# Kernel optimization log

Hardware: AMD Instinct MI355X
Metric: run time of the kernel (lower is better)

## Reference

```python
import jax, jax.numpy as jnp
import numpy as np

B, S, D, H = 2, 2048, 1024, 16
HD = D // H  # head depth


def setup_inputs() -> dict:
    key = jax.random.key(0)
    ks = jax.random.split(key, 8)
    scale = 0.02
    K = jax.random.normal(ks[0], (B, S, D), jnp.float32)
    V = jax.random.normal(ks[1], (B, S, D), jnp.float32)
    Q = jax.random.normal(ks[2], (B, S, D), jnp.float32)
    # causal additive mask: 1.0 where attention is disallowed (strict upper triangle)
    mask = jnp.broadcast_to(
        jnp.triu(jnp.ones((S, S), jnp.float32), k=1)[None, None, :, :], (B, 1, S, S)
    )
    Wk = jax.random.normal(ks[3], (D, D), jnp.float32) * scale
    Wv = jax.random.normal(ks[4], (D, D), jnp.float32) * scale
    Wq = jax.random.normal(ks[5], (D, D), jnp.float32) * scale
    Wo = jax.random.normal(ks[6], (D, D), jnp.float32) * scale
    z = jnp.zeros((D,), jnp.float32)
    return {"K": K, "V": V, "Q": Q, "mask": mask,
            "Wk": Wk, "bk": z, "Wv": Wv, "bv": z,
            "Wq": Wq, "bq": z, "Wo": Wo, "bo": z}


def _split_heads(x):  # [B,S,D] -> [B,H,S,HD]
    return x.reshape(B, S, H, HD).transpose(0, 2, 1, 3)


def reference(K, V, Q, mask, Wk, bk, Wv, bv, Wq, bq, Wo, bo):
    k = _split_heads(K @ Wk + bk)
    v = _split_heads(V @ Wv + bv)
    q = _split_heads(Q @ Wq + bq)
    # NOTE: source scales by sqrt(d_model), not sqrt(head_depth)
    logits = jnp.einsum("bhqd,bhkd->bhqk", q, k) / jnp.sqrt(jnp.float32(D))
    logits = logits + mask * (-1e9)
    attn = jax.nn.softmax(logits, axis=-1)
    out = jnp.einsum("bhqk,bhkd->bhqd", attn, v)  # [B,H,S,HD]
    out = out.transpose(0, 2, 1, 3).reshape(B, S, D)
    return out @ Wo + bo
```

## Files before the change

### kernel.cpp

```cpp
#include <hip/hip_runtime.h>
#include <hip/hip_bf16.h>

typedef unsigned short u16;
typedef unsigned int u32;
typedef unsigned long long u64;
typedef __attribute__((ext_vector_type(8))) __bf16 bf16x8;
typedef __attribute__((ext_vector_type(4))) float f32x4;

#define SEQ 2048
#define DM 1024
#define NH 16
#define HDim 64

__device__ __forceinline__ float bf_lo(u32 u) { return __uint_as_float(u << 16); }
__device__ __forceinline__ float bf_hi(u32 u) { return __uint_as_float(u & 0xffff0000u); }
__device__ __forceinline__ u16 f2bf(float f) {
    u32 u = __float_as_uint(f);
    u32 r = (u + 0x7fffu + ((u >> 16) & 1u)) >> 16;
    return (u16)r;
}
__device__ __forceinline__ float bf2f(u16 h) { return __uint_as_float(((u32)h) << 16); }

__device__ __forceinline__ float fexp2(float x) {
#if __has_builtin(__builtin_amdgcn_exp2f)
    return __builtin_amdgcn_exp2f(x);
#else
    return __expf(x * 0.69314718056f);
#endif
}

__device__ __forceinline__ float frcp(float x) {
#if __has_builtin(__builtin_amdgcn_rcpf)
    return __builtin_amdgcn_rcpf(x);
#else
    return 1.0f / x;
#endif
}

__device__ __forceinline__ u32 merge2(u32 a, u32 b, float inv) {
    const float lo = (bf_lo(a) + bf_lo(b)) * inv;
    const float hi = (bf_hi(a) + bf_hi(b)) * inv;
    u32 r;
    asm("v_cvt_pk_bf16_f32 %0, %1, %2" : "=v"(r) : "v"(lo), "v"(hi));
    return r;
}

#define GLD16(g, l)                                                         \
    __builtin_amdgcn_global_load_lds(                                       \
        (const __attribute__((address_space(1))) void*)(g),                 \
        (__attribute__((address_space(3))) void*)(l), 16, 0, 0)

__device__ __forceinline__ bool detect_f32(const u32* q)
{
    const u32 w = q[threadIdx.x & 63];
    const int e0 = ((w & 0xffffu) >> 7) & 0xff;
    const int e1 = (w >> 23) & 0xff;
    const unsigned long long b = __ballot(e0 >= 0x90 || e1 >= 0x90);
    return b != 0ull;
}

__global__ __launch_bounds__(256)
void prep_all(const void* __restrict__ Qin, const void* __restrict__ Kin,
              const void* __restrict__ Vin,
              const void* __restrict__ w0, const void* __restrict__ w1,
              const void* __restrict__ w2, const void* __restrict__ w3,
              const void* __restrict__ b0, const void* __restrict__ b1,
              const void* __restrict__ b2, const void* __restrict__ b3,
              u16* __restrict__ Xall, u16* __restrict__ Wtall,
              u16* __restrict__ ball)
{
    __shared__ u16 T[64 * 66];
    const bool f = detect_f32((const u32*)Qin);
    const int t = threadIdx.x;
    const int bid = blockIdx.x;

    if (bid < 6144) {
        const int z = bid >> 11;
        const int bx = bid & 2047;
        const void* src = (z == 0) ? Qin : (z == 1) ? Kin : Vin;
        const size_t i0 = ((size_t)bx * 256 + t) * 8;
        u16* d = Xall + (size_t)z * 4194304 + i0;
        if (f) {
            const uint4* s = reinterpret_cast<const uint4*>((const float*)src + i0);
            uint4 a = s[0], b = s[1];
            u16 o[8];
            o[0] = f2bf(__uint_as_float(a.x)); o[1] = f2bf(__uint_as_float(a.y));
            o[2] = f2bf(__uint_as_float(a.z)); o[3] = f2bf(__uint_as_float(a.w));
            o[4] = f2bf(__uint_as_float(b.x)); o[5] = f2bf(__uint_as_float(b.y));
            o[6] = f2bf(__uint_as_float(b.z)); o[7] = f2bf(__uint_as_float(b.w));
            *reinterpret_cast<uint4*>(d) = *reinterpret_cast<const uint4*>(o);
        } else {
            *reinterpret_cast<uint4*>(d) =
                *reinterpret_cast<const uint4*>((const u16*)src + i0);
        }
    } else if (bid < 7168) {
        const int r = bid - 6144;
        const int z = r >> 8;
        const void* src = (z == 0) ? w0 : (z == 1) ? w1 : (z == 2) ? w2 : w3;
        const int n0 = ((r >> 4) & 15) * 64;
        const int k0 = (r & 15) * 64;
        const int c = t & 63, g = t >> 6;
        if (f) {
            const float* W = (const float*)src;
#pragma unroll
            for (int i = 0; i < 16; i++) {
                const int kl = g * 16 + i;
                T[kl * 66 + c] = f2bf(W[(size_t)(k0 + kl) * DM + n0 + c]);
            }
        } else {
            const u16* W = (const u16*)src;
#pragma unroll
            for (int i = 0; i < 16; i++) {
                const int kl = g * 16 + i;
                T[kl * 66 + c] = W[(size_t)(k0 + kl) * DM + n0 + c];
            }
        }
        __syncthreads();
        u16* dst = Wtall + (size_t)z * 1048576;
#pragma unroll
        for (int i = 0; i < 16; i++) {
            const int nl = g * 16 + i;
            dst[(size_t)(n0 + nl) * DM + k0 + c] = T[c * 66 + nl];
        }
    } else {
#pragma unroll
        for (int j = 0; j < 16; j++) {
            const int idx = t * 16 + j;
            const int z = idx >> 10, e = idx & 1023;
            const void* src = (z == 0) ? b0 : (z == 1) ? b1 : (z == 2) ? b2 : b3;
            ball[idx] = f ? f2bf(((const float*)src)[e]) : ((const u16*)src)[e];
        }
    }
}

__global__ __launch_bounds__(256)
void gemm128(const u16* __restrict__ Xall, const u16* __restrict__ Wtall,
             const u16* __restrict__ ball, u16* __restrict__ Yall)
{
    __shared__ __align__(16) u16 As[2][128 * 32];
    __shared__ __align__(16) u16 Bs[2][64 * 32];

    const int zz = blockIdx.z;
    const bool swp = (zz != 2);
    const u16* X  = Xall + (size_t)zz * 4194304;
    const u16* Wt = Wtall + (size_t)zz * 1048576;

    const int t    = threadIdx.x;
    const int w    = t >> 6;
    const int lane = t & 63;
    const int quad = lane >> 4;
    const int ln   = lane & 15;
    const int m0   = blockIdx.x * 128;
    const int n0   = blockIdx.y * 64;

    f32x4 acc[4][2];
#pragma unroll
    for (int i = 0; i < 4; i++)
#pragma unroll
        for (int j = 0; j < 2; j++) acc[i][j] = (f32x4){0.f, 0.f, 0.f, 0.f};

    const int swz = (lane >> 3) & 3;
    const u16* ag = X  + (size_t)(m0 + w * 32 + (lane >> 2)) * DM + ((lane & 3) ^ swz) * 8;
    const u16* bg = Wt + (size_t)(n0 + w * 16 + (lane >> 2)) * DM + ((lane & 3) ^ swz) * 8;

    const int wr = (w >> 1) * 64;
    const int wc = (w & 1) * 32;
    const int rs = (quad ^ ((ln >> 1) & 3)) * 8;

#define GSTAGE(B)                                        \
    {                                                    \
        GLD16(ag,           &As[B][w * 1024]);           \
        GLD16(ag + 16 * DM, &As[B][w * 1024 + 512]);     \
        GLD16(bg,           &Bs[B][w * 512]);            \
        ag += 32; bg += 32;                              \
    }

#define GCOMP(B)                                                              \
    {                                                                         \
        bf16x8 af[4], bfr[2];                                                 \
        _Pragma("unroll") for (int rt = 0; rt < 4; rt++)                      \
            af[rt] = *reinterpret_cast<const bf16x8*>(                        \
                &As[B][(wr + rt * 16 + ln) * 32 + rs]);                       \
        _Pragma("unroll") for (int ct = 0; ct < 2; ct++)                      \
            bfr[ct] = *reinterpret_cast<const bf16x8*>(                       \
                &Bs[B][(wc + ct * 16 + ln) * 32 + rs]);                       \
        if (swp) {                                                            \
            _Pragma("unroll") for (int rt = 0; rt < 4; rt++)                  \
                _Pragma("unroll") for (int ct = 0; ct < 2; ct++)              \
                    acc[rt][ct] = __builtin_amdgcn_mfma_f32_16x16x32_bf16(    \
                        bfr[ct], af[rt], acc[rt][ct], 0, 0, 0);               \
        } else {                                                              \
            _Pragma("unroll") for (int rt = 0; rt < 4; rt++)                  \
                _Pragma("unroll") for (int ct = 0; ct < 2; ct++)              \
                    acc[rt][ct] = __builtin_amdgcn_mfma_f32_16x16x32_bf16(    \
                        af[rt], bfr[ct], acc[rt][ct], 0, 0, 0);               \
        }                                                                     \
    }

    GSTAGE(0);
    __syncthreads();
#pragma unroll 1
    for (int it = 0; it < 15; ++it) {
        GSTAGE(1); GCOMP(0); __syncthreads();
        GSTAGE(0); GCOMP(1); __syncthreads();
    }
    GSTAGE(1); GCOMP(0); __syncthreads();
    GCOMP(1);
#undef GSTAGE
#undef GCOMP

    u16* Y = Yall + (size_t)zz * 4194304;

    if (swp) {
        const float scale = (zz == 0) ? 0.04508422f : 1.0f;
#pragma unroll
        for (int ct = 0; ct < 2; ct++) {
            const int nb = n0 + wc + ct * 16 + quad * 4;
            const int h = nb >> 6, hd = nb & (HDim - 1);
            float bv[4];
#pragma unroll
            for (int r = 0; r < 4; r++) bv[r] = bf2f(ball[zz * 1024 + nb + r]);
#pragma unroll
            for (int rt = 0; rt < 4; rt++) {
                const int m = m0 + wr + rt * 16 + ln;
                const int b = m >> 11, s = m & (SEQ - 1);
                u16 o4[4];
#pragma unroll
                for (int r = 0; r < 4; r++)
                    o4[r] = f2bf((acc[rt][ct][r] + bv[r]) * scale);
                *reinterpret_cast<u64*>(
                    Y + (((size_t)(b * NH + h)) * SEQ + s) * HDim + hd) =
                    *reinterpret_cast<const u64*>(o4);
            }
        }
    } else {
#pragma unroll
        for (int ct = 0; ct < 2; ct++) {
            const int n = n0 + wc + ct * 16 + ln;
            const float bv = bf2f(ball[zz * 1024 + n]);
            const int h = n >> 6, hd = n & (HDim - 1);
#pragma unroll
            for (int rt = 0; rt < 4; rt++) {
                const int m = m0 + wr + rt * 16 + quad * 4;
                const int b = m >> 11, s = m & (SEQ - 1);
                u16 o4[4];
#pragma unroll
                for (int r = 0; r < 4; r++) o4[r] = f2bf(acc[rt][ct][r] + bv);
                *reinterpret_cast<u64*>(
                    Y + (((size_t)(b * NH + h) * HDim + hd) * SEQ + s)) =
                    *reinterpret_cast<const u64*>(o4);
            }
        }
    }
}

__device__ __forceinline__ void attn_tile2(
    const u16* __restrict__ Ks, const u16* __restrict__ Vs,
    u16* __restrict__ Ps, const bf16x8& qf0, const bf16x8& qf1,
    int kt, int qrow, int w, int quad, int ln, f32x4* o, float& l,
    bool diag)
{
    f32x4 s[4];
    __builtin_amdgcn_s_setprio(1);
#pragma unroll
    for (int ct = 0; ct < 4; ct++) {
        const u16* kr = &Ks[(ct * 16 + ln) * 72 + quad * 8];
        bf16x8 kf0 = *reinterpret_cast<const bf16x8*>(kr);
        bf16x8 kf1 = *reinterpret_cast<const bf16x8*>(kr + 32);
        f32x4 z = (f32x4){0.f, 0.f, 0.f, 0.f};
        z = __builtin_amdgcn_mfma_f32_16x16x32_bf16(kf0, qf0, z, 0, 0, 0);
        s[ct] = __builtin_amdgcn_mfma_f32_16x16x32_bf16(kf1, qf1, z, 0, 0, 0);
    }
    __builtin_amdgcn_s_setprio(0);
    const int kb = kt * 64 + quad * 4;
    float lacc = 0.f;
#pragma unroll
    for (int ct = 0; ct < 4; ct++) {
        float e0 = fexp2(s[ct][0]);
        float e1 = fexp2(s[ct][1]);
        float e2 = fexp2(s[ct][2]);
        float e3 = fexp2(s[ct][3]);
        if (diag) {
            const int kc = kb + ct * 16;
            e0 = (kc + 0 <= qrow) ? e0 : 0.f;
            e1 = (kc + 1 <= qrow) ? e1 : 0.f;
            e2 = (kc + 2 <= qrow) ? e2 : 0.f;
            e3 = (kc + 3 <= qrow) ? e3 : 0.f;
        }
        lacc += (e0 + e1) + (e2 + e3);
        u32 pk[2];
        asm("v_cvt_pk_bf16_f32 %0, %1, %2" : "=v"(pk[0]) : "v"(e0), "v"(e1));
        asm("v_cvt_pk_bf16_f32 %0, %1, %2" : "=v"(pk[1]) : "v"(e2), "v"(e3));
        *reinterpret_cast<u64*>(&Ps[(w * 16 + ln) * 72 + ct * 16 + quad * 4]) =
            *reinterpret_cast<const u64*>(pk);
    }
    l += lacc;
    __builtin_amdgcn_s_setprio(1);
#pragma unroll
    for (int ks = 0; ks < 2; ks++) {
        bf16x8 pf = *reinterpret_cast<const bf16x8*>(
            &Ps[(w * 16 + ln) * 72 + ks * 32 + quad * 8]);
#pragma unroll
        for (int nt = 0; nt < 4; nt++) {
            bf16x8 vf = *reinterpret_cast<const bf16x8*>(
                &Vs[(nt * 16 + ln) * 72 + ks * 32 + quad * 8]);
            o[nt] = __builtin_amdgcn_mfma_f32_16x16x32_bf16(pf, vf, o[nt], 0, 0, 0);
        }
    }
    __builtin_amdgcn_s_setprio(0);
}

__global__ __launch_bounds__(256)
void attn_split(const u16* __restrict__ qh, const u16* __restrict__ kh,
                const u16* __restrict__ vt, u16* __restrict__ Opart,
                float* __restrict__ Lpart)
{
    __shared__ __align__(16) u16 Ks[64 * 72];
    __shared__ __align__(16) u16 Vs[64 * 72];
    __shared__ __align__(16) u16 Ps[64 * 72];

    const int t    = threadIdx.x;
    const int L    = blockIdx.x + 16 * (blockIdx.y + 32 * blockIdx.z);
    const int xcd  = L & 7;
    const int slot = L >> 3;
    const int bh   = xcd + 8 * (slot >> 5);
    const int rr   = slot & 31;
    const int i    = rr & 15;
    const int c    = rr >> 4;

    const int w    = t >> 6;
    const int lane = t & 63;
    const int quad = lane >> 4;
    const int ln   = lane & 15;
    const int qtH  = 31 - i;
    const int qtL  = i;
    const int m    = (i >= 8) ? 8 : 16 - i;
    const int kt0  = c ? m : 0;
    const int kt1  = c ? (qtH + 1) : m;

    const size_t kbase = (size_t)bh * SEQ * HDim;
    const size_t vbase = (size_t)bh * HDim * SEQ;

    const u16* qrH = qh + kbase + (size_t)(qtH * 64 + w * 16 + ln) * HDim;
    const bf16x8 qfH0 = *reinterpret_cast<const bf16x8*>(qrH + quad * 8);
    const bf16x8 qfH1 = *reinterpret_cast<const bf16x8*>(qrH + 32 + quad * 8);
    const u16* qrL = qh + kbase + (size_t)(qtL * 64 + w * 16 + ln) * HDim;
    const bf16x8 qfL0 = *reinterpret_cast<const bf16x8*>(qrL + quad * 8);
    const bf16x8 qfL1 = *reinterpret_cast<const bf16x8*>(qrL + 32 + quad * 8);

    f32x4 oH[4], oL[4];
    float lH = 0.f, lL = 0.f;
#pragma unroll
    for (int k = 0; k < 4; k++) {
        oH[k] = (f32x4){0.f, 0.f, 0.f, 0.f};
        oL[k] = (f32x4){0.f, 0.f, 0.f, 0.f};
    }

    const int srow = t >> 2;
    const int sc   = (t & 3) * 16;
    const int rowH = qtH * 64 + w * 16 + ln;
    const int rowL = qtL * 64 + w * 16 + ln;

    uint4 kr0, kr1, vr0, vr1;
    {
        const uint4* ksp = reinterpret_cast<const uint4*>(
            kh + kbase + (size_t)(kt0 * 64 + srow) * HDim + sc);
        kr0 = ksp[0]; kr1 = ksp[1];
        const uint4* vsp = reinterpret_cast<const uint4*>(
            vt + vbase + (size_t)srow * SEQ + kt0 * 64 + sc);
        vr0 = vsp[0]; vr1 = vsp[1];
    }

    for (int kt = kt0; kt < kt1; kt++) {
        {
            uint4* kd = reinterpret_cast<uint4*>(&Ks[srow * 72 + sc]);
            kd[0] = kr0; kd[1] = kr1;
            uint4* vd = reinterpret_cast<uint4*>(&Vs[srow * 72 + sc]);
            vd[0] = vr0; vd[1] = vr1;
        }
        __syncthreads();

        if (kt + 1 < kt1) {
            const uint4* ksp = reinterpret_cast<const uint4*>(
                kh + kbase + (size_t)((kt + 1) * 64 + srow) * HDim + sc);
            kr0 = ksp[0]; kr1 = ksp[1];
            const uint4* vsp = reinterpret_cast<const uint4*>(
                vt + vbase + (size_t)srow * SEQ + (kt + 1) * 64 + sc);
            vr0 = vsp[0]; vr1 = vsp[1];
            __builtin_amdgcn_sched_barrier(0);
        }

        attn_tile2(Ks, Vs, Ps, qfH0, qfH1, kt, rowH, w, quad, ln, oH, lH,
                   kt == qtH);
        if (kt <= qtL)
            attn_tile2(Ks, Vs, Ps, qfL0, qfL1, kt, rowL, w, quad, ln, oL, lL,
                       kt == qtL);

        __syncthreads();
    }

    lH += __shfl_xor(lH, 16); lH += __shfl_xor(lH, 32);
    lL += __shfl_xor(lL, 16); lL += __shfl_xor(lL, 32);

    const size_t cb = ((size_t)c * 32 + bh) * SEQ;
    if (lane < 16) {
        Lpart[cb + qtH * 64 + w * 16 + lane] = lH;
        Lpart[cb + qtL * 64 + w * 16 + lane] = lL;
    }
#pragma unroll
    for (int r = 0; r < 4; r++) {
        const int rH = qtH * 64 + w * 16 + quad * 4 + r;
        const int rL = qtL * 64 + w * 16 + quad * 4 + r;
        u16* dH = Opart + (cb + rH) * HDim + ln;
        u16* dL = Opart + (cb + rL) * HDim + ln;
#pragma unroll
        for (int nt = 0; nt < 4; nt++) {
            dH[nt * 16] = f2bf(oH[nt][r]);
            dL[nt * 16] = f2bf(oL[nt][r]);
        }
    }
}

__global__ __launch_bounds__(256)
void gemm_out(const u16* __restrict__ Opart, const float* __restrict__ Lpart,
              const u16* __restrict__ Wt, const u16* __restrict__ bias,
              void* __restrict__ dout, const u32* __restrict__ qdet)
{
    __shared__ __align__(16) u16 As[2][64 * 32];
    __shared__ __align__(16) u16 Bs[2][64 * 32];

    const size_t CSTR = (size_t)32 * SEQ * HDim;

    const int t    = threadIdx.x;
    const int w    = t >> 6;
    const int lane = t & 63;
    const int quad = lane >> 4;
    const int ln   = lane & 15;
    const int m0   = blockIdx.x * 64;
    const int n0   = blockIdx.y * 64;

    f32x4 acc[2][2];
#pragma unroll
    for (int i = 0; i < 2; i++)
#pragma unroll
        for (int j = 0; j < 2; j++) acc[i][j] = (f32x4){0.f, 0.f, 0.f, 0.f};

    const int swzA = (t >> 3) & 3;
    const int g8   = ((t & 3) ^ swzA) * 8;
    const int r1   = m0 + (t >> 2);
    const int b16  = (r1 >> 11) * 16;
    const int s1   = r1 & (SEQ - 1);
    const int swzB = (lane >> 3) & 3;
    const u16* bg = Wt + (size_t)(n0 + w * 16 + (lane >> 2)) * DM
                       + ((lane & 3) ^ swzB) * 8;

    const int wr = (w >> 1) * 32;
    const int wc = (w & 1) * 32;
    const int rs = (quad ^ ((ln >> 1) & 3)) * 8;

    uint4 pa0, pa1;
    float inv1;

#define OALOAD(kk)                                                            \
    {                                                                         \
        const int col = (kk) + g8;                                            \
        const int bh  = b16 + (col >> 6);                                     \
        const int hd  = col & 63;                                             \
        const size_t e1 = ((size_t)bh * SEQ + s1) * HDim + hd;                \
        pa0 = *reinterpret_cast<const uint4*>(Opart + e1);                    \
        pa1 = *reinterpret_cast<const uint4*>(Opart + CSTR + e1);             \
        inv1 = frcp(Lpart[(size_t)bh * SEQ + s1] +                            \
                    Lpart[(size_t)(32 + bh) * SEQ + s1]);                     \
    }

#define OAWRITE(B)                                                            \
    {                                                                         \
        u32 o[4];                                                             \
        o[0] = merge2(pa0.x, pa1.x, inv1); o[1] = merge2(pa0.y, pa1.y, inv1); \
        o[2] = merge2(pa0.z, pa1.z, inv1); o[3] = merge2(pa0.w, pa1.w, inv1); \
        *reinterpret_cast<uint4*>(&As[B][t * 8]) =                            \
            *reinterpret_cast<const uint4*>(o);                               \
    }

#define OBSTAGE(B)                                       \
    {                                                    \
        GLD16(bg, &Bs[B][w * 512]);                      \
        bg += 32;                                        \
    }

#define OCOMP(B)                                                              \
    {                                                                         \
        bf16x8 af[2], bfr[2];                                                 \
        _Pragma("unroll") for (int rt = 0; rt < 2; rt++)                      \
            af[rt] = *reinterpret_cast<const bf16x8*>(                        \
                &As[B][(wr + rt * 16 + ln) * 32 + rs]);                       \
        _Pragma("unroll") for (int ct = 0; ct < 2; ct++)                      \
            bfr[ct] = *reinterpret_cast<const bf16x8*>(                       \
                &Bs[B][(wc + ct * 16 + ln) * 32 + rs]);                       \
        _Pragma("unroll") for (int rt = 0; rt < 2; rt++)                      \
            _Pragma("unroll") for (int ct = 0; ct < 2; ct++)                  \
                acc[rt][ct] = __builtin_amdgcn_mfma_f32_16x16x32_bf16(        \
                    af[rt], bfr[ct], acc[rt][ct], 0, 0, 0);                   \
    }

    OALOAD(0); OBSTAGE(0); OAWRITE(0);
    __syncthreads();
    int kk = 32;
#pragma unroll 1
    for (int it = 0; it < 15; ++it) {
        OALOAD(kk); OBSTAGE(1); OCOMP(0); OAWRITE(1);
        __syncthreads();
        kk += 32;
        OALOAD(kk); OBSTAGE(0); OCOMP(1); OAWRITE(0);
        __syncthreads();
        kk += 32;
    }
    OALOAD(kk); OBSTAGE(1); OCOMP(0); OAWRITE(1);
    __syncthreads();
    OCOMP(1);
#undef OALOAD
#undef OAWRITE
#undef OBSTAGE
#undef OCOMP

    const bool f = detect_f32(qdet);
#pragma unroll
    for (int ct = 0; ct < 2; ct++) {
        const int n = n0 + wc + ct * 16 + ln;
        const float bv = bf2f(bias[n]);
#pragma unroll
        for (int rt = 0; rt < 2; rt++) {
            const int mb = m0 + wr + rt * 16 + quad * 4;
#pragma unroll
            for (int r = 0; r < 4; r++) {
                const float val = acc[rt][ct][r] + bv;
                if (f) ((float*)dout)[(size_t)(mb + r) * DM + n] = val;
                else   ((u16*)dout)[(size_t)(mb + r) * DM + n] = f2bf(val);
            }
        }
    }
}

__global__ __launch_bounds__(64)
void detect_dtype(const u32* __restrict__ q, int* __restrict__ flag)
{
    const int t = threadIdx.x;
    const u32 w = q[t];
    const int e0 = ((w & 0xffffu) >> 7) & 0xff;
    const int e1 = (w >> 23) & 0xff;
    const unsigned long long b = __ballot(e0 >= 0x90 || e1 >= 0x90);
    if (t == 0) *flag = (b != 0ull) ? 1 : 0;
}

struct AttnAcc { f32x4 o[4]; float l[4]; };

__device__ __forceinline__ void attn_tile(
    const u16* __restrict__ Ks, const u16* __restrict__ Vs,
    u16* __restrict__ Ps, const bf16x8& qf0, const bf16x8& qf1,
    int kt, int rowb, int w, int quad, int ln, AttnAcc& a)
{
    f32x4 s[4];
#pragma unroll
    for (int ct = 0; ct < 4; ct++) {
        const u16* kr = &Ks[(ct * 16 + ln) * 72 + quad * 8];
        bf16x8 kf0 = *reinterpret_cast<const bf16x8*>(kr);
        bf16x8 kf1 = *reinterpret_cast<const bf16x8*>(kr + 32);
        f32x4 z = (f32x4){0.f, 0.f, 0.f, 0.f};
        z = __builtin_amdgcn_mfma_f32_16x16x32_bf16(qf0, kf0, z, 0, 0, 0);
        s[ct] = __builtin_amdgcn_mfma_f32_16x16x32_bf16(qf1, kf1, z, 0, 0, 0);
    }
#pragma unroll
    for (int ct = 0; ct < 4; ct++) {
        const int kcol = kt * 64 + ct * 16 + ln;
#pragma unroll
        for (int r = 0; r < 4; r++) {
            const float e = (kcol <= rowb + r) ? __expf(s[ct][r]) : 0.f;
            a.l[r] += e;
            Ps[(w * 16 + quad * 4 + r) * 68 + ct * 16 + ln] = f2bf(e);
        }
    }
#pragma unroll
    for (int ks = 0; ks < 2; ks++) {
        bf16x8 pf = *reinterpret_cast<const bf16x8*>(
            &Ps[(w * 16 + ln) * 68 + ks * 32 + quad * 8]);
#pragma unroll
        for (int nt = 0; nt < 4; nt++) {
            bf16x8 vf = *reinterpret_cast<const bf16x8*>(
                &Vs[(nt * 16 + ln) * 72 + ks * 32 + quad * 8]);
            a.o[nt] = __builtin_amdgcn_mfma_f32_16x16x32_bf16(pf, vf, a.o[nt], 0, 0, 0);
        }
    }
}

__global__ __launch_bounds__(256)
void attn_mfma(const u16* __restrict__ qh, const u16* __restrict__ kh,
               const u16* __restrict__ vt, u16* __restrict__ ctx)
{
    __shared__ __align__(16) u16 Ks[64 * 72];
    __shared__ __align__(16) u16 Vs[64 * 72];
    __shared__ __align__(16) u16 Ps[64 * 68];

    const int t    = threadIdx.x;
    const int i    = blockIdx.x;
    const int bh   = blockIdx.y;
    const int w    = t >> 6;
    const int lane = t & 63;
    const int quad = lane >> 4;
    const int ln   = lane & 15;
    const int qtH  = 31 - i;
    const int qtL  = i;

    const size_t kbase = (size_t)bh * SEQ * HDim;
    const size_t vbase = (size_t)bh * HDim * SEQ;

    const u16* qrH = qh + kbase + (size_t)(qtH * 64 + w * 16 + ln) * HDim;
    const bf16x8 qfH0 = *reinterpret_cast<const bf16x8*>(qrH + quad * 8);
    const bf16x8 qfH1 = *reinterpret_cast<const bf16x8*>(qrH + 32 + quad * 8);
    const u16* qrL = qh + kbase + (size_t)(qtL * 64 + w * 16 + ln) * HDim;
    const bf16x8 qfL0 = *reinterpret_cast<const bf16x8*>(qrL + quad * 8);
    const bf16x8 qfL1 = *reinterpret_cast<const bf16x8*>(qrL + 32 + quad * 8);

    AttnAcc aH, aL;
#pragma unroll
    for (int k = 0; k < 4; k++) {
        aH.o[k] = (f32x4){0.f, 0.f, 0.f, 0.f}; aH.l[k] = 0.f;
        aL.o[k] = (f32x4){0.f, 0.f, 0.f, 0.f}; aL.l[k] = 0.f;
    }

    const int srow = t >> 2;
    const int sc   = (t & 3) * 16;
    const int rowHb = qtH * 64 + w * 16 + quad * 4;
    const int rowLb = qtL * 64 + w * 16 + quad * 4;

    for (int kt = 0; kt <= qtH; kt++) {
        {
            const uint4* ks = reinterpret_cast<const uint4*>(
                kh + kbase + (size_t)(kt * 64 + srow) * HDim + sc);
            uint4* kd = reinterpret_cast<uint4*>(&Ks[srow * 72 + sc]);
            kd[0] = ks[0];
            kd[1] = ks[1];
            const uint4* vs = reinterpret_cast<const uint4*>(
                vt + vbase + (size_t)srow * SEQ + kt * 64 + sc);
            uint4* vd = reinterpret_cast<uint4*>(&Vs[srow * 72 + sc]);
            vd[0] = vs[0];
            vd[1] = vs[1];
        }
        __syncthreads();

        attn_tile(Ks, Vs, Ps, qfH0, qfH1, kt, rowHb, w, quad, ln, aH);
        if (kt <= qtL)
            attn_tile(Ks, Vs, Ps, qfL0, qfL1, kt, rowLb, w, quad, ln, aL);

        __syncthreads();
    }

#pragma unroll
    for (int m = 1; m < 16; m <<= 1) {
#pragma unroll
        for (int r = 0; r < 4; r++) {
            aH.l[r] += __shfl_xor(aH.l[r], m);
            aL.l[r] += __shfl_xor(aL.l[r], m);
        }
    }

    const int b = bh >> 4;
    const int h = bh & 15;
#pragma unroll
    for (int r = 0; r < 4; r++) {
        const float invH = 1.f / aH.l[r];
        const float invL = 1.f / aL.l[r];
        const int sH = qtH * 64 + w * 16 + quad * 4 + r;
        const int sL = qtL * 64 + w * 16 + quad * 4 + r;
        u16* dH = ctx + ((size_t)(b * SEQ + sH)) * DM + h * HDim + ln;
        u16* dL = ctx + ((size_t)(b * SEQ + sL)) * DM + h * HDim + ln;
#pragma unroll
        for (int nt = 0; nt < 4; nt++) {
            dH[nt * 16] = f2bf(aH.o[nt][r] * invH);
            dL[nt * 16] = f2bf(aL.o[nt][r] * invL);
        }
    }
}

__global__ __launch_bounds__(256)
void gemm_bias(const void* __restrict__ Xv, const void* __restrict__ Wv,
               const void* __restrict__ biasv, void* __restrict__ Yv,
               int M, int N, int K, int mode, int xsel, int wsel, int ysel,
               float scale, const int* __restrict__ flagp)
{
    __shared__ __align__(16) u16 As[64 * 32];
    __shared__ __align__(16) u16 Bs[64 * 40];

    const int f  = *flagp;
    const bool xf = (xsel != 0) && (f != 0);
    const bool wf = (wsel != 0) && (f != 0);
    const bool yf = (ysel != 0) && (f != 0);

    const u16*   Xb = (const u16*)Xv;
    const float* Xf = (const float*)Xv;
    const u16*   Wb = (const u16*)Wv;
    const float* Wf = (const float*)Wv;

    const int t    = threadIdx.x;
    const int m0   = blockIdx.y * 64;
    const int n0   = blockIdx.x * 64;
    const int w    = t >> 6;
    const int lane = t & 63;
    const int quad = lane >> 4;
    const int ln   = lane & 15;

    f32x4 acc[4];
#pragma unroll
    for (int i = 0; i < 4; i++) acc[i] = (f32x4){0.f, 0.f, 0.f, 0.f};

    const int a_row = t >> 2;
    const int a_c8  = (t & 3) * 8;
    const int b_n   = t & 63;
    const int b_k8  = (t >> 6) * 8;

    for (int kk = 0; kk < K; kk += 32) {
        const size_t aoff = (size_t)(m0 + a_row) * K + kk + a_c8;
        if (!xf) {
            *reinterpret_cast<uint4*>(&As[a_row * 32 + a_c8]) =
                *reinterpret_cast<const uint4*>(Xb + aoff);
        } else {
            const float* src = Xf + aoff;
            uint4 u0 = reinterpret_cast<const uint4*>(src)[0];
            uint4 u1 = reinterpret_cast<const uint4*>(src)[1];
            u16 tmp[8];
            tmp[0] = f2bf(__uint_as_float(u0.x));
            tmp[1] = f2bf(__uint_as_float(u0.y));
            tmp[2] = f2bf(__uint_as_float(u0.z));
            tmp[3] = f2bf(__uint_as_float(u0.w));
            tmp[4] = f2bf(__uint_as_float(u1.x));
            tmp[5] = f2bf(__uint_as_float(u1.y));
            tmp[6] = f2bf(__uint_as_float(u1.z));
            tmp[7] = f2bf(__uint_as_float(u1.w));
            *reinterpret_cast<uint4*>(&As[a_row * 32 + a_c8]) =
                *reinterpret_cast<const uint4*>(tmp);
        }
        u16 tmp[8];
        if (!wf) {
#pragma unroll
            for (int j = 0; j < 8; j++)
                tmp[j] = Wb[(size_t)(kk + b_k8 + j) * N + n0 + b_n];
        } else {
#pragma unroll
            for (int j = 0; j < 8; j++)
                tmp[j] = f2bf(Wf[(size_t)(kk + b_k8 + j) * N + n0 + b_n]);
        }
        *reinterpret_cast<uint4*>(&Bs[b_n * 40 + b_k8]) =
            *reinterpret_cast<const uint4*>(tmp);

        __syncthreads();

        bf16x8 bfrag = *reinterpret_cast<const bf16x8*>(&Bs[(w * 16 + ln) * 40 + quad * 8]);
#pragma unroll
        for (int rt = 0; rt < 4; rt++) {
            bf16x8 afrag = *reinterpret_cast<const bf16x8*>(&As[(rt * 16 + ln) * 32 + quad * 8]);
            acc[rt] = __builtin_amdgcn_mfma_f32_16x16x32_bf16(afrag, bfrag, acc[rt], 0, 0, 0);
        }
        __syncthreads();
    }

    const int n = n0 + w * 16 + ln;
    const float bv = wf ? ((const float*)biasv)[n] : bf2f(((const u16*)biasv)[n]);
#pragma unroll
    for (int rt = 0; rt < 4; rt++) {
        if (mode == 2) {
            const int m = m0 + rt * 16 + quad * 4;
            const int b = m >> 11;
            const int s = m & (SEQ - 1);
            const int h = n >> 6;
            const int hd = n & (HDim - 1);
            u16 o4[4];
#pragma unroll
            for (int r = 0; r < 4; r++) o4[r] = f2bf((acc[rt][r] + bv) * scale);
            *reinterpret_cast<u64*>(
                (u16*)Yv + (((size_t)(b * NH + h) * HDim + hd) * SEQ + s)) =
                *reinterpret_cast<const u64*>(o4);
        } else {
#pragma unroll
            for (int r = 0; r < 4; r++) {
                const int m = m0 + rt * 16 + quad * 4 + r;
                const float val = (acc[rt][r] + bv) * scale;
                if (mode == 0) {
                    if (yf) ((float*)Yv)[(size_t)m * N + n] = val;
                    else    ((u16*)Yv)[(size_t)m * N + n] = f2bf(val);
                } else {
                    const int b = m >> 11;
                    const int s = m & (SEQ - 1);
                    const int h = n >> 6;
                    const int hd = n & (HDim - 1);
                    ((u16*)Yv)[(((size_t)(b * NH + h)) * SEQ + s) * HDim + hd] = f2bf(val);
                }
            }
        }
    }
}

extern "C" void kernel_launch(void* const* d_in, const int* in_sizes, int n_in,
                              void* d_out, int out_size, void* d_ws, size_t ws_size,
                              hipStream_t stream)
{
    const void* Kin = d_in[0];
    const void* Vin = d_in[1];
    const void* Qin = d_in[2];
    const void* Wk = d_in[4];
    const void* bk = d_in[5];
    const void* Wv = d_in[6];
    const void* bv = d_in[7];
    const void* Wq = d_in[8];
    const void* bq = d_in[9];
    const void* Wo = d_in[10];
    const void* bo = d_in[11];

    char* ws = (char*)d_ws;
    const size_t NEED = ((size_t)29360128 + 4096) * 2 + 256;

    if (ws_size >= NEED) {
        u16* Xall  = (u16*)ws;
        u16* Yall  = (u16*)ws + 12582912;
        u16* Wtall = (u16*)ws + 25165824;
        u16* ball  = (u16*)ws + 29360128;
        u16* qhp   = Yall;
        u16* khp   = Yall + 4194304;
        u16* vtp   = Yall + 8388608;
        u16* Opart = Xall + 4194304;
        float* Lpart = (float*)Wtall;

        hipLaunchKernelGGL(prep_all, dim3(7169), dim3(256), 0, stream,
                           Qin, Kin, Vin, Wq, Wk, Wv, Wo, bq, bk, bv, bo,
                           Xall, Wtall, ball);

        hipLaunchKernelGGL(gemm128, dim3(32, 16, 3), dim3(256), 0, stream,
                           Xall, Wtall, ball, Yall);

        hipLaunchKernelGGL(attn_split, dim3(16, 32, 2), dim3(256), 0, stream,
                           qhp, khp, vtp, Opart, Lpart);

        hipLaunchKernelGGL(gemm_out, dim3(64, 16), dim3(256), 0, stream,
                           Opart, Lpart, Wtall + (size_t)3 * 1048576,
                           ball + 3 * 1024, d_out, (const u32*)Qin);
    } else {
        const size_t SEG = (size_t)2 * SEQ * DM * sizeof(u16);
        u16* qh  = (u16*)(ws);
        u16* khd = (u16*)(ws + SEG);
        u16* vtd = (u16*)(ws + 2 * SEG);
        u16* ctx = (u16*)(ws + 3 * SEG);
        int* flag = (int*)(ws + 4 * SEG);

        hipLaunchKernelGGL(detect_dtype, dim3(1), dim3(64), 0, stream,
                           (const u32*)Qin, flag);

        const int M = 2 * SEQ;
        dim3 ggrid(DM / 64, M / 64);
        dim3 gblk(256);

        hipLaunchKernelGGL(gemm_bias, ggrid, gblk, 0, stream, Qin, Wq, bq, qh,  M, DM, DM, 1, 1, 1, 0, 0.03125f, flag);
        hipLaunchKernelGGL(gemm_bias, ggrid, gblk, 0, stream, Kin, Wk, bk, khd, M, DM, DM, 1, 1, 1, 0, 1.0f,     flag);
        hipLaunchKernelGGL(gemm_bias, ggrid, gblk, 0, stream, Vin, Wv, bv, vtd, M, DM, DM, 2, 1, 1, 0, 1.0f,     flag);

        hipLaunchKernelGGL(attn_mfma, dim3(16, 2 * NH), dim3(256), 0,
                           stream, qh, khd, vtd, ctx);

        hipLaunchKernelGGL(gemm_bias, ggrid, gblk, 0, stream, ctx, Wo, bo, d_out, M, DM, DM, 0, 0, 1, 1, 1.0f, flag);
    }
}
```

Measured before the change: 256.0 us.

## Fuse fp32-to-bf16 input conversion into projection GEMM A-tile loading

Drops the separate pass that converted the Q/K/V activations to bf16 in workspace. The projection GEMM now reads fp32 inputs directly into registers, packs them to bf16 and writes them into shared memory, overlapping with the MFMA compute of the other buffer. This removes one full write and re-read of the activations plus that part of the prep kernel. The cost is that the GEMM fetches twice as many A bytes per tile, and the A path uses register loads instead of direct-to-LDS loads, which adds VGPR pressure and conversion instructions to the inner loop.

```diff
diff --git a/kernel.cpp b/kernel.cpp
--- a/kernel.cpp
+++ b/kernel.cpp
@@ -37,12 +37,14 @@
 #endif
 }
 
+__device__ __forceinline__ u32 pk2(float a, float b) {
+    u32 r;
+    asm("v_cvt_pk_bf16_f32 %0, %1, %2" : "=v"(r) : "v"(a), "v"(b));
+    return r;
+}
+
 __device__ __forceinline__ u32 merge2(u32 a, u32 b, float inv) {
-    const float lo = (bf_lo(a) + bf_lo(b)) * inv;
-    const float hi = (bf_hi(a) + bf_hi(b)) * inv;
-    u32 r;
-    asm("v_cvt_pk_bf16_f32 %0, %1, %2" : "=v"(r) : "v"(lo), "v"(hi));
-    return r;
+    return pk2((bf_lo(a) + bf_lo(b)) * inv, (bf_hi(a) + bf_hi(b)) * inv);
 }
 
 #define GLD16(g, l)                                                         \
@@ -60,41 +62,20 @@
 }
 
 __global__ __launch_bounds__(256)
-void prep_all(const void* __restrict__ Qin, const void* __restrict__ Kin,
-              const void* __restrict__ Vin,
+void prep_all(const void* __restrict__ Qin,
               const void* __restrict__ w0, const void* __restrict__ w1,
               const void* __restrict__ w2, const void* __restrict__ w3,
               const void* __restrict__ b0, const void* __restrict__ b1,
               const void* __restrict__ b2, const void* __restrict__ b3,
-              u16* __restrict__ Xall, u16* __restrict__ Wtall,
-              u16* __restrict__ ball)
+              u16* __restrict__ Wtall, u16* __restrict__ ball)
 {
     __shared__ u16 T[64 * 66];
     const bool f = detect_f32((const u32*)Qin);
     const int t = threadIdx.x;
     const int bid = blockIdx.x;
 
-    if (bid < 6144) {
-        const int z = bid >> 11;
-        const int bx = bid & 2047;
-        const void* src = (z == 0) ? Qin : (z == 1) ? Kin : Vin;
-        const size_t i0 = ((size_t)bx * 256 + t) * 8;
-        u16* d = Xall + (size_t)z * 4194304 + i0;
-        if (f) {
-            const uint4* s = reinterpret_cast<const uint4*>((const float*)src + i0);
-            uint4 a = s[0], b = s[1];
-            u16 o[8];
-            o[0] = f2bf(__uint_as_float(a.x)); o[1] = f2bf(__uint_as_float(a.y));
-            o[2] = f2bf(__uint_as_float(a.z)); o[3] = f2bf(__uint_as_float(a.w));
-            o[4] = f2bf(__uint_as_float(b.x)); o[5] = f2bf(__uint_as_float(b.y));
-            o[6] = f2bf(__uint_as_float(b.z)); o[7] = f2bf(__uint_as_float(b.w));
-            *reinterpret_cast<uint4*>(d) = *reinterpret_cast<const uint4*>(o);
-        } else {
-            *reinterpret_cast<uint4*>(d) =
-                *reinterpret_cast<const uint4*>((const u16*)src + i0);
-        }
-    } else if (bid < 7168) {
-        const int r = bid - 6144;
+    if (bid < 1024) {
+        const int r = bid;
         const int z = r >> 8;
         const void* src = (z == 0) ? w0 : (z == 1) ? w1 : (z == 2) ? w2 : w3;
         const int n0 = ((r >> 4) & 15) * 64;
@@ -134,16 +115,19 @@
 }
 
 __global__ __launch_bounds__(256)
-void gemm128(const u16* __restrict__ Xall, const u16* __restrict__ Wtall,
-             const u16* __restrict__ ball, u16* __restrict__ Yall)
+void gemm128(const void* __restrict__ Qin, const void* __restrict__ Kin,
+             const void* __restrict__ Vin,
+             const u16* __restrict__ Wtall, const u16* __restrict__ ball,
+             u16* __restrict__ Yall)
 {
     __shared__ __align__(16) u16 As[2][128 * 32];
     __shared__ __align__(16) u16 Bs[2][64 * 32];
 
     const int zz = blockIdx.z;
     const bool swp = (zz != 2);
-    const u16* X  = Xall + (size_t)zz * 4194304;
+    const void* Xsrc = (zz == 0) ? Qin : (zz == 1) ? Kin : Vin;
     const u16* Wt = Wtall + (size_t)zz * 1048576;
+    const bool xf = detect_f32((const u32*)Qin);
 
     const int t    = threadIdx.x;
     const int w    = t >> 6;
@@ -159,20 +143,57 @@
 #pragma unroll
         for (int j = 0; j < 2; j++) acc[i][j] = (f32x4){0.f, 0.f, 0.f, 0.f};
 
-    const int swz = (lane >> 3) & 3;
-    const u16* ag = X  + (size_t)(m0 + w * 32 + (lane >> 2)) * DM + ((lane & 3) ^ swz) * 8;
-    const u16* bg = Wt + (size_t)(n0 + w * 16 + (lane >> 2)) * DM + ((lane & 3) ^ swz) * 8;
+    const int swz  = (lane >> 3) & 3;
+    const int acol = ((lane & 3) ^ swz) * 8;
+    const size_t aoff = (size_t)(m0 + w * 32 + (lane >> 2)) * DM + acol;
+    const float* agf = (const float*)Xsrc + aoff;
+    const u16*   agb = (const u16*)Xsrc + aoff;
+    const u16* bg = Wt + (size_t)(n0 + w * 16 + (lane >> 2)) * DM + acol;
 
     const int wr = (w >> 1) * 64;
     const int wc = (w & 1) * 32;
     const int rs = (quad ^ ((ln >> 1) & 3)) * 8;
 
-#define GSTAGE(B)                                        \
+    uint4 a0, a1, a2, a3;
+
+#define ALOAD()                                                 \
+    {                                                           \
+        if (xf) {                                               \
+            a0 = *reinterpret_cast<const uint4*>(agf);          \
+            a1 = *reinterpret_cast<const uint4*>(agf + 4);      \
+            a2 = *reinterpret_cast<const uint4*>(agf + 16 * DM);\
+            a3 = *reinterpret_cast<const uint4*>(agf + 16 * DM + 4); \
+            agf += 32;                                          \
+        }                                                       \
+    }
+
+#define AWRITE(B)                                                            \
+    {                                                                        \
+        if (xf) {                                                            \
+            u32 o[4];                                                        \
+            o[0] = pk2(__uint_as_float(a0.x), __uint_as_float(a0.y));        \
+            o[1] = pk2(__uint_as_float(a0.z), __uint_as_float(a0.w));        \
+            o[2] = pk2(__uint_as_float(a1.x), __uint_as_float(a1.y));        \
+            o[3] = pk2(__uint_as_float(a1.z), __uint_as_float(a1.w));        \
+            *reinterpret_cast<uint4*>(&As[B][w * 1024 + lane * 8]) =         \
+                *reinterpret_cast<const uint4*>(o);                          \
+            o[0] = pk2(__uint_as_float(a2.x), __uint_as_float(a2.y));        \
+            o[1] = pk2(__uint_as_float(a2.z), __uint_as_float(a2.w));        \
+            o[2] = pk2(__uint_as_float(a3.x), __uint_as_float(a3.y));        \
+            o[3] = pk2(__uint_as_float(a3.z), __uint_as_float(a3.w));        \
+            *reinterpret_cast<uint4*>(&As[B][w * 1024 + 512 + lane * 8]) =   \
+                *reinterpret_cast<const uint4*>(o);                          \
+        } else {                                                             \
+            GLD16(agb,           &As[B][w * 1024]);                          \
+            GLD16(agb + 16 * DM, &As[B][w * 1024 + 512]);                    \
+            agb += 32;                                                       \
+        }                                                                    \
+    }
+
+#define BSTAGE(B)                                        \
     {                                                    \
-        GLD16(ag,           &As[B][w * 1024]);           \
-        GLD16(ag + 16 * DM, &As[B][w * 1024 + 512]);     \
-        GLD16(bg,           &Bs[B][w * 512]);            \
-        ag += 32; bg += 32;                              \
+        GLD16(bg, &Bs[B][w * 512]);                      \
+        bg += 32;                                        \
     }
 
 #define GCOMP(B)                                                              \
@@ -197,16 +218,21 @@
         }                                                                     \
     }
 
-    GSTAGE(0);
+    ALOAD(); BSTAGE(0); AWRITE(0);
     __syncthreads();
 #pragma unroll 1
     for (int it = 0; it < 15; ++it) {
-        GSTAGE(1); GCOMP(0); __syncthreads();
-        GSTAGE(0); GCOMP(1); __syncthreads();
-    }
-    GSTAGE(1); GCOMP(0); __syncthreads();
+        ALOAD(); BSTAGE(1); GCOMP(0); AWRITE(1);
+        __syncthreads();
+        ALOAD(); BSTAGE(0); GCOMP(1); AWRITE(0);
+        __syncthreads();
+    }
+    ALOAD(); BSTAGE(1); GCOMP(0); AWRITE(1);
+    __syncthreads();
     GCOMP(1);
-#undef GSTAGE
+#undef ALOAD
+#undef AWRITE
+#undef BSTAGE
 #undef GCOMP
 
     u16* Y = Yall + (size_t)zz * 4194304;
@@ -289,8 +315,8 @@
         }
         lacc += (e0 + e1) + (e2 + e3);
         u32 pk[2];
-        asm("v_cvt_pk_bf16_f32 %0, %1, %2" : "=v"(pk[0]) : "v"(e0), "v"(e1));
-        asm("v_cvt_pk_bf16_f32 %0, %1, %2" : "=v"(pk[1]) : "v"(e2), "v"(e3));
+        pk[0] = pk2(e0, e1);
+        pk[1] = pk2(e2, e3);
         *reinterpret_cast<u64*>(&Ps[(w * 16 + ln) * 72 + ct * 16 + quad * 4]) =
             *reinterpret_cast<const u64*>(pk);
     }
@@ -828,12 +854,12 @@
         u16* Opart = Xall + 4194304;
         float* Lpart = (float*)Wtall;
 
-        hipLaunchKernelGGL(prep_all, dim3(7169), dim3(256), 0, stream,
-                           Qin, Kin, Vin, Wq, Wk, Wv, Wo, bq, bk, bv, bo,
-                           Xall, Wtall, ball);
+        hipLaunchKernelGGL(prep_all, dim3(1025), dim3(256), 0, stream,
+                           Qin, Wq, Wk, Wv, Wo, bq, bk, bv, bo,
+                           Wtall, ball);
 
         hipLaunchKernelGGL(gemm128, dim3(32, 16, 3), dim3(256), 0, stream,
-                           Xall, Wtall, ball, Yall);
+                           Qin, Kin, Vin, Wtall, ball, Yall);
 
         hipLaunchKernelGGL(attn_split, dim3(16, 32, 2), dim3(256), 0, stream,
                            qhp, khp, vtp, Opart, Lpart);
```

Measured after the change: 278.7 us. 1.09x slower.
